# Performance work log

Measured on AMD Instinct MI355X. Metric: run time of the kernel, lower is better.

The kernel has to match this reference:

```python
import jax, jax.numpy as jnp
import numpy as np

D = 256; N_GRU = 4; L = 3; RATIO = 0.8; B = 64; PAD = 0
VOCAB = 50000; N = 20000; E = 320000; T = 16


def setup_inputs() -> dict:
    key = jax.random.key(0)
    ks = jax.random.split(key, 10)
    s = 0.05
    return {
        "x_tokens": jax.random.randint(ks[0], (N, T), 0, VOCAB),
        "edge_index": jax.random.randint(ks[1], (2, E), 0, N),
        "batch": jnp.sort(jax.random.randint(ks[2], (N,), 0, B)),
        "embed": jax.random.normal(ks[3], (VOCAB, D)) * s,
        "ggc_W": jax.random.normal(ks[4], (L, N_GRU, D, D)) * s,
        "gru_Wih": jax.random.normal(ks[5], (L, 3 * D, D)) * s,
        "gru_Whh": jax.random.normal(ks[6], (L, 3 * D, D)) * s,
        "gru_bih": jnp.zeros((L, 3 * D)),
        "gru_bhh": jnp.zeros((L, 3 * D)),
        "topk_p": jax.random.normal(ks[7], (L, D)) * s,
        "gate_W": jax.random.normal(ks[8], (D, 1)) * s,
        "gate_b": jnp.zeros((1,)),
    }


def gru_cell(m, h, Wih, Whh, bih, bhh):
    gi = m @ Wih.T + bih
    gh = h @ Whh.T + bhh
    i_r, i_z, i_n = jnp.split(gi, 3, axis=-1)
    h_r, h_z, h_n = jnp.split(gh, 3, axis=-1)
    r = jax.nn.sigmoid(i_r + h_r)
    z = jax.nn.sigmoid(i_z + h_z)
    n = jnp.tanh(i_n + r * h_n)
    return (1.0 - z) * n + z * h


def gated_graph_conv(h, src, dst, emask, W, Wih, Whh, bih, bhh):
    # PyG GatedGraphConv: per step, transform then scatter-add source->target, then GRU update
    for l in range(N_GRU):
        msg = (h @ W[l])[src] * emask[:, None]            # [E, D]
        agg = jax.ops.segment_sum(msg, dst, num_segments=h.shape[0])
        h = gru_cell(agg, h, Wih, Whh, bih, bhh)
    return h


def topk_pool(x, p, nmask, batch, src, dst, emask):
    # PyG TopKPooling: score = tanh(x.p/||p||), keep top ceil(ratio*n) per graph, x *= score
    score = jnp.tanh((x @ p) / jnp.linalg.norm(p))
    skey = jnp.where(nmask, score, -1e9)
    order = jnp.lexsort((-skey, batch))                   # by graph asc, score desc
    counts = jax.ops.segment_sum(jnp.ones((N,), jnp.int32), batch, num_segments=B)
    starts = jnp.cumsum(counts) - counts
    rank = jnp.zeros((N,), jnp.int32).at[order].set(
        jnp.arange(N, dtype=jnp.int32) - starts[batch[order]])
    n_valid = jax.ops.segment_sum(nmask.astype(jnp.int32), batch, num_segments=B)
    k = jnp.ceil(RATIO * n_valid.astype(jnp.float32)).astype(jnp.int32)
    keep = nmask & (rank < k[batch])
    x_new = jnp.where(keep[:, None], x * score[:, None], 0.0)
    emask_new = emask * keep[src].astype(emask.dtype) * keep[dst].astype(emask.dtype)
    return x_new, keep, emask_new


def global_att(x, nmask, batch, gW, gb):
    # GlobalAttention: segment softmax of Linear(x,1), weighted sum per graph
    logit = jnp.where(nmask, (x @ gW)[:, 0] + gb[0], -1e9)
    mx = jax.ops.segment_max(logit, batch, num_segments=B)
    e = jnp.where(nmask, jnp.exp(logit - mx[batch]), 0.0)
    denom = jax.ops.segment_sum(e, batch, num_segments=B)
    gate = e / jnp.maximum(denom[batch], 1e-12)
    return jax.ops.segment_sum(gate[:, None] * x, batch, num_segments=B)


def reference(x_tokens, edge_index, batch, embed, ggc_W, gru_Wih, gru_Whh,
              gru_bih, gru_bhh, topk_p, gate_W, gate_b):
    # STEncoder: embed token ids, mean-pool non-pad tokens per node
    tok_mask = (x_tokens != PAD)
    emb = embed[x_tokens] * tok_mask[..., None]
    h = emb.sum(1) / jnp.maximum(tok_mask.sum(1, keepdims=True), 1).astype(emb.dtype)
    src, dst = edge_index[0], edge_index[1]
    nmask = jnp.ones((N,), bool)
    emask = jnp.ones((E,), h.dtype)
    out = jnp.zeros((B, D), h.dtype)
    for l in range(L):
        h = jax.nn.relu(gated_graph_conv(h, src, dst, emask, ggc_W[l],
                                         gru_Wih[l], gru_Whh[l], gru_bih[l], gru_bhh[l]))
        h, nmask, emask = topk_pool(h, topk_p[l], nmask, batch, src, dst, emask)
        out = out + global_att(h, nmask, batch, gate_W, gate_b)
    return out
```

## Files before the change

### kernel.cpp

```cpp
#include <hip/hip_runtime.h>
#include <hip/hip_bf16.h>

namespace {

constexpr int NN = 20000;
constexpr int TT = 16;
constexpr int DD = 256;
constexpr int EE = 320000;
constexpr int BB = 64;
constexpr int NLAY = 3;
constexpr int NGRUS = 4;
constexpr int D3 = 768;
constexpr int NRB = 157;
constexpr int NXCD = 8;

typedef __bf16 bf16x8 __attribute__((ext_vector_type(8)));
typedef float  f32x4  __attribute__((ext_vector_type(4)));

__device__ __forceinline__ float us2f(unsigned short u){
  union { unsigned int i; float f; } v; v.i = ((unsigned int)u) << 16; return v.f;
}
__device__ __forceinline__ unsigned short f2us(float f){
  union { float f; unsigned int i; } v; v.f = f;
  unsigned int r = v.i + 0x7fff + ((v.i >> 16) & 1);
  return (unsigned short)(r >> 16);
}

__device__ __forceinline__ void gload16(const unsigned short* g, unsigned short* l){
  __builtin_amdgcn_global_load_lds(
      (const __attribute__((address_space(1))) unsigned int*)g,
      (__attribute__((address_space(3))) unsigned int*)l, 16, 0, 0);
}

__global__ void k_init(int* __restrict__ deg, int* __restrict__ cursor,
                       int* __restrict__ nmask, float* __restrict__ out){
  int i = blockIdx.x*256 + threadIdx.x;
  if (i < NN){ deg[i] = 0; cursor[i] = 0; nmask[i] = 1; }
  if (i < BB*DD) out[i] = 0.f;
}

__global__ void k_embed(const int* __restrict__ xt, const float* __restrict__ emb,
                        unsigned short* __restrict__ h){
  int n = blockIdx.x; int d = threadIdx.x;
  __shared__ int toks[TT];
  if (threadIdx.x < TT) toks[threadIdx.x] = xt[n*TT + threadIdx.x];
  __syncthreads();
  float acc = 0.f; int cnt = 0;
  #pragma unroll
  for (int t = 0; t < TT; ++t){
    int tk = toks[t];
    if (tk != 0){ ++cnt; acc += emb[(size_t)tk*DD + d]; }
  }
  h[(size_t)n*DD + d] = f2us(acc / (float)(cnt > 0 ? cnt : 1));
}

__global__ __launch_bounds__(256) void k_wf(const float* __restrict__ W,
                                            const float* __restrict__ Wih,
                                            unsigned short* __restrict__ WFThi,
                                            unsigned short* __restrict__ WFTlo){
  int lg = blockIdx.z; int l = lg / NGRUS;
  const float* A  = W   + (size_t)lg*DD*DD;
  const float* Bm = Wih + (size_t)l*D3*DD;
  unsigned short* oh = WFThi + (size_t)lg*D3*DD;
  unsigned short* ol = WFTlo + (size_t)lg*D3*DD;
  int k0 = blockIdx.y*64, j0 = blockIdx.x*64;
  __shared__ float sA[16][68], sB[16][68];
  int tid = threadIdx.x, ty = tid/16, tx = tid%16;
  float acc[4][4] = {};
  int m = tid >> 2, dg = (tid & 3)*4;
  for (int d0 = 0; d0 < DD; d0 += 16){
    float4 ua = *reinterpret_cast<const float4*>(A  + (size_t)(k0+m)*DD + d0+dg);
    float4 ub = *reinterpret_cast<const float4*>(Bm + (size_t)(j0+m)*DD + d0+dg);
    __syncthreads();
    sA[dg+0][m]=ua.x; sA[dg+1][m]=ua.y; sA[dg+2][m]=ua.z; sA[dg+3][m]=ua.w;
    sB[dg+0][m]=ub.x; sB[dg+1][m]=ub.y; sB[dg+2][m]=ub.z; sB[dg+3][m]=ub.w;
    __syncthreads();
    #pragma unroll
    for (int dd = 0; dd < 16; ++dd){
      float a[4], b[4];
      #pragma unroll
      for (int i=0;i<4;++i) a[i] = sA[dd][ty*4+i];
      #pragma unroll
      for (int j=0;j<4;++j) b[j] = sB[dd][tx*4+j];
      #pragma unroll
      for (int i=0;i<4;++i)
        #pragma unroll
        for (int j=0;j<4;++j) acc[i][j] += a[i]*b[j];
    }
  }
  for (int i=0;i<4;++i){
    int k = k0 + ty*4 + i;
    for (int j=0;j<4;++j){
      int c = j0 + tx*4 + j;
      float v = acc[i][j];
      unsigned short hi = f2us(v);
      float rem = v - us2f(hi);
      oh[(size_t)c*DD + k] = hi;
      ol[(size_t)c*DD + k] = f2us(rem);
    }
  }
}

__global__ void k_whh_split(const float* __restrict__ Whh, unsigned short* __restrict__ hi,
                            unsigned short* __restrict__ lo){
  size_t i = (size_t)blockIdx.x*256 + threadIdx.x;
  if (i >= (size_t)NLAY*D3*DD) return;
  float w = Whh[i];
  unsigned short h = f2us(w);
  hi[i] = h; lo[i] = f2us(w - us2f(h));
}

__global__ void k_deg(const int* __restrict__ dst, int* __restrict__ deg){
  int e = blockIdx.x*256 + threadIdx.x; if (e < EE) atomicAdd(&deg[dst[e]], 1);
}
__global__ void k_scan(const int* __restrict__ deg, int* __restrict__ offs){
  __shared__ int part[1024];
  int t = threadIdx.x; const int CH = 20;
  int base = t*CH; int s = 0;
  for (int i = 0; i < CH; ++i){ int idx = base+i; if (idx < NN) s += deg[idx]; }
  part[t] = s; __syncthreads();
  for (int o = 1; o < 1024; o <<= 1){
    int v = part[t]; int add = (t >= o) ? part[t-o] : 0;
    __syncthreads(); part[t] = v + add; __syncthreads();
  }
  int run = (t > 0) ? part[t-1] : 0;
  for (int i = 0; i < CH; ++i){ int idx = base+i; if (idx < NN){ offs[idx] = run; run += deg[idx]; } }
  if (t == 1023) offs[NN] = run;
}
__global__ void k_fill_csr(const int* __restrict__ src, const int* __restrict__ dst,
                           const int* __restrict__ offs, int* __restrict__ cursor,
                           int* __restrict__ csr_src){
  int e = blockIdx.x*256 + threadIdx.x; if (e >= EE) return;
  int d = dst[e]; int pos = atomicAdd(&cursor[d], 1);
  csr_src[offs[d] + pos] = src[e];
}

__global__ void k_bounds(const int* __restrict__ batch, int* __restrict__ starts65){
  int n = blockIdx.x*256 + threadIdx.x;
  if (n >= NN) return;
  int b = batch[n];
  int p = (n == 0) ? -1 : batch[n-1];
  for (int bb = p+1; bb <= b; ++bb) starts65[bb] = n;
  if (n == NN-1){
    for (int bb = b+1; bb <= BB; ++bb) starts65[bb] = NN;
  }
}
__global__ void k_cnts(const int* __restrict__ starts65, int* __restrict__ counts){
  int b = threadIdx.x;
  if (b < BB) counts[b] = starts65[b+1] - starts65[b];
}

__global__ void k_agg(const unsigned short* __restrict__ h, const int* __restrict__ offs,
                      const int* __restrict__ csr_src, unsigned short* __restrict__ agg){
  int wid = threadIdx.x >> 6, lane = threadIdx.x & 63;
  int n = blockIdx.x*4 + wid;
  if (n >= NN) return;
  int s = offs[n], e = offs[n+1];
  float a0 = 0.f, a1 = 0.f, a2 = 0.f, a3 = 0.f;
  for (int base = s; base < e; base += 64){
    int cnt = min(64, e - base);
    int idx = (lane < cnt) ? csr_src[base + lane] : 0;
    int i = 0;
    for (; i + 4 <= cnt; i += 4){
      int s0 = __shfl(idx, i+0), s1 = __shfl(idx, i+1);
      int s2 = __shfl(idx, i+2), s3 = __shfl(idx, i+3);
      ushort4 v0 = *reinterpret_cast<const ushort4*>(h + (size_t)s0*DD + lane*4);
      ushort4 v1 = *reinterpret_cast<const ushort4*>(h + (size_t)s1*DD + lane*4);
      ushort4 v2 = *reinterpret_cast<const ushort4*>(h + (size_t)s2*DD + lane*4);
      ushort4 v3 = *reinterpret_cast<const ushort4*>(h + (size_t)s3*DD + lane*4);
      a0 += us2f(v0.x); a1 += us2f(v0.y); a2 += us2f(v0.z); a3 += us2f(v0.w);
      a0 += us2f(v1.x); a1 += us2f(v1.y); a2 += us2f(v1.z); a3 += us2f(v1.w);
      a0 += us2f(v2.x); a1 += us2f(v2.y); a2 += us2f(v2.z); a3 += us2f(v2.w);
      a0 += us2f(v3.x); a1 += us2f(v3.y); a2 += us2f(v3.z); a3 += us2f(v3.w);
    }
    for (; i < cnt; ++i){
      int s0 = __shfl(idx, i);
      ushort4 v0 = *reinterpret_cast<const ushort4*>(h + (size_t)s0*DD + lane*4);
      a0 += us2f(v0.x); a1 += us2f(v0.y); a2 += us2f(v0.z); a3 += us2f(v0.w);
    }
  }
  ushort4 o;
  o.x = f2us(a0); o.y = f2us(a1); o.z = f2us(a2); o.w = f2us(a3);
  *reinterpret_cast<ushort4*>(agg + (size_t)n*DD + lane*4) = o;
}

__global__ __launch_bounds__(256) void k_gru(
    const unsigned short* __restrict__ Ag, const unsigned short* __restrict__ Ah,
    const unsigned short* __restrict__ WfH, const unsigned short* __restrict__ WfL,
    const unsigned short* __restrict__ WhH, const unsigned short* __restrict__ WhL,
    const float* __restrict__ bih, const float* __restrict__ bhh,
    const int* __restrict__ nmask, unsigned short* __restrict__ Hn, int do_relu){
  __shared__ unsigned short sB[2][96*64];
  int t = threadIdx.x;
  int wv = t >> 6, lane = t & 63;
  int lr = lane & 15, kg = lane >> 4;

  int w = blockIdx.x;
  int q = (w & 7)*NRB + (w >> 3);
  int r0 = (q >> 3) * 128;
  int g0 = q & 7;

  int sw   = ((lane & 7) ^ (lane >> 3)) * 8;
  int rloc = lane >> 3;

  auto stageB = [&](int buf, int p){
    int a = p >> 1;
    const unsigned short* m = (p & 1) ? ((a & 4) ? WhL : WfL)
                                      : ((a & 4) ? WhH : WfH);
    int kin0 = (a & 3) * 64;
    #pragma unroll
    for (int i = 0; i < 3; ++i){
      int brow = (wv + i*4)*8;
      int gate = brow >> 5;
      int srcrow = gate*256 + g0*32 + (brow & 31) + rloc;
      gload16(m + (size_t)srcrow*DD + kin0 + sw, &sB[buf][brow*64]);
    }
  };

  f32x4 aR[2][2], aZ[2][2], aNi[2][2], aNh[2][2];
  #pragma unroll
  for (int rf = 0; rf < 2; ++rf)
    #pragma unroll
    for (int h2 = 0; h2 < 2; ++h2){
      aR[rf][h2] = (f32x4){0.f,0.f,0.f,0.f};  aZ[rf][h2] = (f32x4){0.f,0.f,0.f,0.f};
      aNi[rf][h2] = (f32x4){0.f,0.f,0.f,0.f}; aNh[rf][h2] = (f32x4){0.f,0.f,0.f,0.f};
    }

  size_t arow0 = (size_t)(r0 + wv*32 + lr) * DD;
  size_t arow1 = (size_t)(r0 + wv*32 + 16 + lr) * DD;

  stageB(0, 0);
  #pragma unroll
  for (int a = 0; a < 8; ++a){
    const unsigned short* Asrc = (a & 4) ? Ah : Ag;
    int kin0 = (a & 3) * 64;
    bf16x8 aF0[2], aF1[2];
    #pragma unroll
    for (int kk2 = 0; kk2 < 2; ++kk2){
      aF0[kk2] = *reinterpret_cast<const bf16x8*>(Asrc + arow0 + kin0 + kk2*32 + kg*8);
      aF1[kk2] = *reinterpret_cast<const bf16x8*>(Asrc + arow1 + kin0 + kk2*32 + kg*8);
    }
    int half = (a >> 2) & 1;
    #pragma unroll
    for (int ph = 0; ph < 2; ++ph){
      int p = a*2 + ph;
      int bbuf = p & 1;
      __syncthreads();
      if (p < 15) stageB(bbuf ^ 1, p + 1);
      __builtin_amdgcn_s_setprio(1);
      #pragma unroll
      for (int kk2 = 0; kk2 < 2; ++kk2){
        int cs = ((kk2*4 + kg) ^ (lr & 7)) * 8;
        bf16x8 a0 = aF0[kk2];
        bf16x8 a1 = aF1[kk2];
        #pragma unroll
        for (int h2 = 0; h2 < 2; ++h2){
          bf16x8 bR = *reinterpret_cast<const bf16x8*>(&sB[bbuf][(      h2*16 + lr)*64 + cs]);
          bf16x8 bZ = *reinterpret_cast<const bf16x8*>(&sB[bbuf][(32  + h2*16 + lr)*64 + cs]);
          bf16x8 bN = *reinterpret_cast<const bf16x8*>(&sB[bbuf][(64  + h2*16 + lr)*64 + cs]);
          aR[0][h2] = __builtin_amdgcn_mfma_f32_16x16x32_bf16(a0, bR, aR[0][h2], 0, 0, 0);
          aR[1][h2] = __builtin_amdgcn_mfma_f32_16x16x32_bf16(a1, bR, aR[1][h2], 0, 0, 0);
          aZ[0][h2] = __builtin_amdgcn_mfma_f32_16x16x32_bf16(a0, bZ, aZ[0][h2], 0, 0, 0);
          aZ[1][h2] = __builtin_amdgcn_mfma_f32_16x16x32_bf16(a1, bZ, aZ[1][h2], 0, 0, 0);
          if (half){
            aNh[0][h2] = __builtin_amdgcn_mfma_f32_16x16x32_bf16(a0, bN, aNh[0][h2], 0, 0, 0);
            aNh[1][h2] = __builtin_amdgcn_mfma_f32_16x16x32_bf16(a1, bN, aNh[1][h2], 0, 0, 0);
          } else {
            aNi[0][h2] = __builtin_amdgcn_mfma_f32_16x16x32_bf16(a0, bN, aNi[0][h2], 0, 0, 0);
            aNi[1][h2] = __builtin_amdgcn_mfma_f32_16x16x32_bf16(a1, bN, aNi[1][h2], 0, 0, 0);
          }
        }
      }
      __builtin_amdgcn_s_setprio(0);
    }
  }

  #pragma unroll
  for (int h2 = 0; h2 < 2; ++h2){
    int col = g0*32 + h2*16 + lr;
    float bRv = bih[col]       + bhh[col];
    float bZv = bih[256 + col] + bhh[256 + col];
    float bN1 = bih[512 + col];
    float bN2 = bhh[512 + col];
    #pragma unroll
    for (int rf = 0; rf < 2; ++rf){
      #pragma unroll
      for (int j = 0; j < 4; ++j){
        int row = r0 + wv*32 + rf*16 + kg*4 + j;
        if (row < NN){
          float r = 1.f/(1.f + expf(-(aR[rf][h2][j] + bRv)));
          float z = 1.f/(1.f + expf(-(aZ[rf][h2][j] + bZv)));
          float nv = tanhf(aNi[rf][h2][j] + bN1 + r*(aNh[rf][h2][j] + bN2));
          float ho = us2f(Ah[(size_t)row*DD + col]);
          float o = (1.f - z)*nv + z*ho;
          if (do_relu) o = fmaxf(o, 0.f);
          if (!nmask[row]) o = 0.f;
          Hn[(size_t)row*DD + col] = f2us(o);
        }
      }
    }
  }
}

__global__ void k_score(const unsigned short* __restrict__ h, const float* __restrict__ p,
                        float* __restrict__ score){
  int wid = threadIdx.x >> 6, lane = threadIdx.x & 63;
  int n = blockIdx.x*4 + wid; if (n >= NN) return;
  ushort4 hu = *reinterpret_cast<const ushort4*>(h + (size_t)n*DD + lane*4);
  float4 pv = *reinterpret_cast<const float4*>(p + lane*4);
  float dot = us2f(hu.x)*pv.x + us2f(hu.y)*pv.y + us2f(hu.z)*pv.z + us2f(hu.w)*pv.w;
  float pp = pv.x*pv.x + pv.y*pv.y + pv.z*pv.z + pv.w*pv.w;
  for (int o = 32; o; o >>= 1){ dot += __shfl_down(dot, o); pp += __shfl_down(pp, o); }
  if (lane == 0) score[n] = tanhf(dot / sqrtf(pp));
}

__global__ void k_topk(const float* __restrict__ score, const int* __restrict__ starts,
                       const int* __restrict__ counts, int* __restrict__ nmask){
  int b = blockIdx.x; int st = starts[b]; int cnt = min(counts[b], 1024);
  __shared__ float sc[1024]; __shared__ int ired[256];
  int t = threadIdx.x;
  int myvalid = 0;
  for (int i = t; i < cnt; i += 256){
    int node = st + i; int v = nmask[node];
    sc[i] = v ? score[node] : -1e30f;
    myvalid += v;
  }
  ired[t] = myvalid; __syncthreads();
  for (int o = 128; o; o >>= 1){ if (t < o) ired[t] += ired[t+o]; __syncthreads(); }
  int nv = ired[0];
  int k = (4*nv + 4)/5;
  __syncthreads();
  for (int i = t; i < cnt; i += 256){
    float si = sc[i]; int node = st + i; int keep = 0;
    if (si > -1e29f){
      int rank = 0;
      for (int j = 0; j < cnt; ++j){
        float sj = sc[j];
        rank += (sj > si) || (sj == si && j < i);
      }
      keep = (rank < k);
    }
    nmask[node] = keep;
  }
}

__global__ void k_scale(unsigned short* __restrict__ h, const float* __restrict__ score,
                        const int* __restrict__ nmask){
  int idx = blockIdx.x*256 + threadIdx.x;
  int n = idx >> 8;
  unsigned short v = nmask[n] ? f2us(us2f(h[idx])*score[n]) : (unsigned short)0;
  h[idx] = v;
}

__global__ void k_att(const unsigned short* __restrict__ h, const float* __restrict__ gW,
                      const float* __restrict__ gb, const int* __restrict__ starts,
                      const int* __restrict__ counts, const int* __restrict__ nmask,
                      float* __restrict__ outacc){
  int b = blockIdx.x; int st = starts[b]; int cnt = min(counts[b], 1024);
  __shared__ float lg[1024]; __shared__ float red[256];
  int t = threadIdx.x, wid = t >> 6, lane = t & 63;
  float gbv = gb[0];
  for (int i = wid; i < cnt; i += 4){
    int node = st + i;
    ushort4 hu = *reinterpret_cast<const ushort4*>(h + (size_t)node*DD + lane*4);
    float4 wv = *reinterpret_cast<const float4*>(gW + lane*4);
    float dot = us2f(hu.x)*wv.x + us2f(hu.y)*wv.y + us2f(hu.z)*wv.z + us2f(hu.w)*wv.w;
    for (int o = 32; o; o >>= 1) dot += __shfl_down(dot, o);
    if (lane == 0) lg[i] = nmask[node] ? dot + gbv : -1e30f;
  }
  __syncthreads();
  float mx = -1e30f;
  for (int i = t; i < cnt; i += 256) mx = fmaxf(mx, lg[i]);
  red[t] = mx; __syncthreads();
  for (int o = 128; o; o >>= 1){ if (t < o) red[t] = fmaxf(red[t], red[t+o]); __syncthreads(); }
  mx = red[0]; __syncthreads();
  float se = 0.f;
  for (int i = t; i < cnt; i += 256){
    float e = (lg[i] > -1e29f) ? expf(lg[i] - mx) : 0.f;
    lg[i] = e; se += e;
  }
  red[t] = se; __syncthreads();
  for (int o = 128; o; o >>= 1){ if (t < o) red[t] += red[t+o]; __syncthreads(); }
  float denom = fmaxf(red[0], 1e-12f);
  __syncthreads();
  float a0=0.f,a1=0.f,a2=0.f,a3=0.f;
  int i = 0;
  for (; i + 4 <= cnt; i += 4){
    a0 += lg[i+0]*us2f(h[(size_t)(st+i+0)*DD + t]);
    a1 += lg[i+1]*us2f(h[(size_t)(st+i+1)*DD + t]);
    a2 += lg[i+2]*us2f(h[(size_t)(st+i+2)*DD + t]);
    a3 += lg[i+3]*us2f(h[(size_t)(st+i+3)*DD + t]);
  }
  for (; i < cnt; ++i) a0 += lg[i]*us2f(h[(size_t)(st+i)*DD + t]);
  outacc[(size_t)b*DD + t] += (a0+a1+a2+a3)/denom;
}

}

extern "C" void kernel_launch(void* const* d_in, const int* in_sizes, int n_in,
                              void* d_out, int out_size, void* d_ws, size_t ws_size,
                              hipStream_t stream){
  const int*   x_tokens = (const int*)d_in[0];
  const int*   e_src    = (const int*)d_in[1];
  const int*   e_dst    = e_src + EE;
  const int*   batch    = (const int*)d_in[2];
  const float* embed    = (const float*)d_in[3];
  const float* ggcW     = (const float*)d_in[4];
  const float* gWih     = (const float*)d_in[5];
  const float* gWhh     = (const float*)d_in[6];
  const float* gbih     = (const float*)d_in[7];
  const float* gbhh     = (const float*)d_in[8];
  const float* topkp    = (const float*)d_in[9];
  const float* gateW    = (const float*)d_in[10];
  const float* gateb    = (const float*)d_in[11];
  (void)in_sizes; (void)n_in; (void)out_size;
  float* out = (float*)d_out;

  char* ws = (char*)d_ws;
  size_t off = 0;
  auto carve = [&](size_t bytes)->char*{
    char* p = ws + off;
    off += (bytes + 255) & ~(size_t)255;
    return p;
  };
  unsigned short* h0    = (unsigned short*)carve((size_t)NN*DD*2);
  unsigned short* h1    = (unsigned short*)carve((size_t)NN*DD*2);
  unsigned short* agg   = (unsigned short*)carve((size_t)NN*DD*2);
  unsigned short* WFThi = (unsigned short*)carve((size_t)NLAY*NGRUS*D3*DD*2);
  unsigned short* WFTlo = (unsigned short*)carve((size_t)NLAY*NGRUS*D3*DD*2);
  unsigned short* WhhHi = (unsigned short*)carve((size_t)NLAY*D3*DD*2);
  unsigned short* WhhLo = (unsigned short*)carve((size_t)NLAY*D3*DD*2);
  float* score   = (float*)carve((size_t)NN*4);
  int* nmask     = (int*)carve((size_t)NN*4);
  int* deg       = (int*)carve((size_t)NN*4);
  int* cursor    = (int*)carve((size_t)NN*4);
  int* offs      = (int*)carve((size_t)(NN+1)*4);
  int* csr_src   = (int*)carve((size_t)EE*4);
  int* counts    = (int*)carve((size_t)BB*4);
  int* starts    = (int*)carve((size_t)(BB+1)*4);
  if (off > ws_size) return;

  k_init<<<(NN+255)/256, 256, 0, stream>>>(deg, cursor, nmask, out);
  k_embed<<<NN, DD, 0, stream>>>(x_tokens, embed, h0);
  k_wf<<<dim3(D3/64, DD/64, NLAY*NGRUS), 256, 0, stream>>>(ggcW, gWih, WFThi, WFTlo);
  k_whh_split<<<(NLAY*D3*DD + 255)/256, 256, 0, stream>>>(gWhh, WhhHi, WhhLo);
  k_deg<<<(EE+255)/256, 256, 0, stream>>>(e_dst, deg);
  k_scan<<<1, 1024, 0, stream>>>(deg, offs);
  k_fill_csr<<<(EE+255)/256, 256, 0, stream>>>(e_src, e_dst, offs, cursor, csr_src);
  k_bounds<<<(NN+255)/256, 256, 0, stream>>>(batch, starts);
  k_cnts<<<1, 64, 0, stream>>>(starts, counts);

  unsigned short* hc = h0; unsigned short* hn = h1;
  for (int l = 0; l < NLAY; ++l){
    const unsigned short* WhHl = WhhHi + (size_t)l*D3*DD;
    const unsigned short* WhLl = WhhLo + (size_t)l*D3*DD;
    const float* bihl = gbih + (size_t)l*D3;
    const float* bhhl = gbhh + (size_t)l*D3;
    for (int g = 0; g < NGRUS; ++g){
      const unsigned short* WfHl = WFThi + (size_t)(l*NGRUS+g)*D3*DD;
      const unsigned short* WfLl = WFTlo + (size_t)(l*NGRUS+g)*D3*DD;
      k_agg<<<(NN+3)/4, 256, 0, stream>>>(hc, offs, csr_src, agg);
      k_gru<<<NRB*NXCD, 256, 0, stream>>>(agg, hc, WfHl, WfLl, WhHl, WhLl,
                                          bihl, bhhl, nmask, hn,
                                          (g == NGRUS-1) ? 1 : 0);
      unsigned short* tmp = hc; hc = hn; hn = tmp;
    }
    k_score<<<NN/4, 256, 0, stream>>>(hc, topkp + (size_t)l*DD, score);
    k_topk<<<BB, 256, 0, stream>>>(score, starts, counts, nmask);
    k_scale<<<NN, 256, 0, stream>>>(hc, score, nmask);
    k_att<<<BB, 256, 0, stream>>>(hc, gateW, gateb, starts, counts, nmask, out);
  }
}
```

Measured before the change: 1.252 ms.

## Prefetch GRU A fragments one step ahead, vectorize embed, add occupancy bound

The GRU MFMA kernel now double-buffers its A-operand register fragments, loading the next K-slice while the current one feeds MFMAs. This hides global load latency that previously stalled the start of each slice. The embedding kernel is rewritten to use one wave per node with float4 loads and shuffle-broadcast tokens instead of a block per node. A launch bound of 4 blocks per SM is added to k_gru, which may force register spills given the doubled fragment registers.

```diff
diff --git a/kernel.cpp b/kernel.cpp
--- a/kernel.cpp
+++ b/kernel.cpp
@@ -41,17 +41,25 @@
 
 __global__ void k_embed(const int* __restrict__ xt, const float* __restrict__ emb,
                         unsigned short* __restrict__ h){
-  int n = blockIdx.x; int d = threadIdx.x;
-  __shared__ int toks[TT];
-  if (threadIdx.x < TT) toks[threadIdx.x] = xt[n*TT + threadIdx.x];
-  __syncthreads();
-  float acc = 0.f; int cnt = 0;
+  int wid = threadIdx.x >> 6, lane = threadIdx.x & 63;
+  int n = blockIdx.x*4 + wid;
+  if (n >= NN) return;
+  int tk = (lane < TT) ? xt[n*TT + lane] : 0;
+  float a0 = 0.f, a1 = 0.f, a2 = 0.f, a3 = 0.f;
+  int cnt = 0;
   #pragma unroll
   for (int t = 0; t < TT; ++t){
-    int tk = toks[t];
-    if (tk != 0){ ++cnt; acc += emb[(size_t)tk*DD + d]; }
-  }
-  h[(size_t)n*DD + d] = f2us(acc / (float)(cnt > 0 ? cnt : 1));
+    int tok = __shfl(tk, t);
+    if (tok != 0){
+      ++cnt;
+      float4 v = *reinterpret_cast<const float4*>(emb + (size_t)tok*DD + lane*4);
+      a0 += v.x; a1 += v.y; a2 += v.z; a3 += v.w;
+    }
+  }
+  float inv = 1.f / (float)(cnt > 0 ? cnt : 1);
+  ushort4 o;
+  o.x = f2us(a0*inv); o.y = f2us(a1*inv); o.z = f2us(a2*inv); o.w = f2us(a3*inv);
+  *reinterpret_cast<ushort4*>(h + (size_t)n*DD + lane*4) = o;
 }
 
 __global__ __launch_bounds__(256) void k_wf(const float* __restrict__ W,
@@ -184,7 +192,7 @@
   *reinterpret_cast<ushort4*>(agg + (size_t)n*DD + lane*4) = o;
 }
 
-__global__ __launch_bounds__(256) void k_gru(
+__global__ __launch_bounds__(256, 4) void k_gru(
     const unsigned short* __restrict__ Ag, const unsigned short* __restrict__ Ah,
     const unsigned short* __restrict__ WfH, const unsigned short* __restrict__ WfL,
     const unsigned short* __restrict__ WhH, const unsigned short* __restrict__ WhL,
@@ -229,17 +237,17 @@
   size_t arow0 = (size_t)(r0 + wv*32 + lr) * DD;
   size_t arow1 = (size_t)(r0 + wv*32 + 16 + lr) * DD;
 
+  bf16x8 aF0[2][2], aF1[2][2];
+  #pragma unroll
+  for (int kk2 = 0; kk2 < 2; ++kk2){
+    aF0[0][kk2] = *reinterpret_cast<const bf16x8*>(Ag + arow0 + kk2*32 + kg*8);
+    aF1[0][kk2] = *reinterpret_cast<const bf16x8*>(Ag + arow1 + kk2*32 + kg*8);
+  }
   stageB(0, 0);
+
   #pragma unroll
   for (int a = 0; a < 8; ++a){
-    const unsigned short* Asrc = (a & 4) ? Ah : Ag;
-    int kin0 = (a & 3) * 64;
-    bf16x8 aF0[2], aF1[2];
-    #pragma unroll
-    for (int kk2 = 0; kk2 < 2; ++kk2){
-      aF0[kk2] = *reinterpret_cast<const bf16x8*>(Asrc + arow0 + kin0 + kk2*32 + kg*8);
-      aF1[kk2] = *reinterpret_cast<const bf16x8*>(Asrc + arow1 + kin0 + kk2*32 + kg*8);
-    }
+    int par = a & 1;
     int half = (a >> 2) & 1;
     #pragma unroll
     for (int ph = 0; ph < 2; ++ph){
@@ -247,12 +255,21 @@
       int bbuf = p & 1;
       __syncthreads();
       if (p < 15) stageB(bbuf ^ 1, p + 1);
+      if (ph == 0 && a < 7){
+        const unsigned short* An = ((a+1) & 4) ? Ah : Ag;
+        int kinn = ((a+1) & 3) * 64;
+        #pragma unroll
+        for (int kk2 = 0; kk2 < 2; ++kk2){
+          aF0[par ^ 1][kk2] = *reinterpret_cast<const bf16x8*>(An + arow0 + kinn + kk2*32 + kg*8);
+          aF1[par ^ 1][kk2] = *reinterpret_cast<const bf16x8*>(An + arow1 + kinn + kk2*32 + kg*8);
+        }
+      }
       __builtin_amdgcn_s_setprio(1);
       #pragma unroll
       for (int kk2 = 0; kk2 < 2; ++kk2){
         int cs = ((kk2*4 + kg) ^ (lr & 7)) * 8;
-        bf16x8 a0 = aF0[kk2];
-        bf16x8 a1 = aF1[kk2];
+        bf16x8 a0 = aF0[par][kk2];
+        bf16x8 a1 = aF1[par][kk2];
         #pragma unroll
         for (int h2 = 0; h2 < 2; ++h2){
           bf16x8 bR = *reinterpret_cast<const bf16x8*>(&sB[bbuf][(      h2*16 + lr)*64 + cs]);
@@ -441,7 +458,7 @@
   if (off > ws_size) return;
 
   k_init<<<(NN+255)/256, 256, 0, stream>>>(deg, cursor, nmask, out);
-  k_embed<<<NN, DD, 0, stream>>>(x_tokens, embed, h0);
+  k_embed<<<(NN+3)/4, 256, 0, stream>>>(x_tokens, embed, h0);
   k_wf<<<dim3(D3/64, DD/64, NLAY*NGRUS), 256, 0, stream>>>(ggcW, gWih, WFThi, WFTlo);
   k_whh_split<<<(NLAY*D3*DD + 255)/256, 256, 0, stream>>>(gWhh, WhhHi, WhhLo);
   k_deg<<<(EE+255)/256, 256, 0, stream>>>(e_dst, deg);
```

Measured after the change: 1.234 ms, median of 2. Within noise of the previous version (-1.4%).
